# Optimization experiments

Measured on AMD Instinct MI355X. Metric: run time of the kernel, lower is better.

Reference implementation:

```python
import jax, jax.numpy as jnp
import numpy as np

EPS = 1e-10

def norm_t(x, axis):
    # zero-mean + L2 normalize along `axis` (standard NCC normalization)
    xc = x - jnp.mean(x, axis=axis, keepdims=True)
    return xc / (jnp.linalg.norm(xc, axis=axis, keepdims=True) + EPS)

def setup_inputs() -> dict:
    key = jax.random.key(0)
    k1, k2 = jax.random.split(key)
    input_compressed = jax.random.normal(k1, (1, 16, 131072), dtype=jnp.float32)  # [B, K, N]
    cmat = jax.random.normal(k2, (16, 1024), dtype=jnp.float32)                   # [K, D]
    return {"input_compressed": input_compressed, "cmat": cmat}

def reference(input_compressed, cmat):
    a = norm_t(input_compressed, axis=-2)          # [B, K, N], normalized over K
    b = norm_t(cmat, axis=0)                       # [K, D],    normalized over K
    ncc = jnp.einsum('bkn,kd->bnd', a, b)          # [B, N, D] correlation volume
    # torch: argmax(transpose(ncc,-2,-1), dim=-2) -> argmax over D -> [B, N]
    pred_depths = jnp.argmax(ncc, axis=-1)         # [B, N] int depth-bin indices
    return pred_depths
```

## Files before the change

kernel.cpp:

```cpp
#include <hip/hip_runtime.h>
#include <hip/hip_bf16.h>
#include <math.h>

#define N_PTS  131072
#define K_DIM  16
#define D_BINS 1024
#define MARGIN 1e-4f

typedef short bf16x8 __attribute__((ext_vector_type(8)));
typedef float f32x4  __attribute__((ext_vector_type(4)));

#define WS_OFF_BN    64
#define WS_OFF_B1    (WS_OFF_BN + 65536)
#define WS_OFF_B2    (WS_OFF_B1 + 32768)
#define WS_OFF_ZERO  (WS_OFF_B2 + 32768)
#define WS_OFF_WL    (WS_OFF_ZERO + 16)
#define WS_NEED      (WS_OFF_WL + 4 * N_PTS)

__device__ __forceinline__ void norm_np(const float* __restrict__ p,
                                        int stride, int n, float* __restrict__ a) {
#pragma clang fp contract(off)
    float v[K_DIM];
#pragma unroll
    for (int k = 0; k < K_DIM; ++k) v[k] = p[(size_t)k * stride + n];
    float s = v[0];
#pragma unroll
    for (int k = 1; k < K_DIM; ++k) s = s + v[k];
    const float mean = s / 16.0f;
    float sq[K_DIM];
#pragma unroll
    for (int k = 0; k < K_DIM; ++k) { a[k] = v[k] - mean; sq[k] = a[k] * a[k]; }
    float ss = sq[0];
#pragma unroll
    for (int k = 1; k < K_DIM; ++k) ss = ss + sq[k];
    const float denom = sqrtf(ss) + 1e-10f;
#pragma unroll
    for (int k = 0; k < K_DIM; ++k) a[k] = a[k] / denom;
}

__device__ __forceinline__ unsigned short bf16_bits(float f) {
    __hip_bfloat16 h = __float2bfloat16(f);
    unsigned short u;
    __builtin_memcpy(&u, &h, 2);
    return u;
}
__device__ __forceinline__ float bf16_val(float f) {
    return __bfloat162float(__float2bfloat16(f));
}

__global__ __launch_bounds__(256) void prep_b(
    const float* __restrict__ cmat, float* __restrict__ bnT,
    unsigned short* __restrict__ B1, unsigned short* __restrict__ B2,
    unsigned short* __restrict__ zblk, int* __restrict__ wl_count) {
#pragma clang fp contract(off)
    if (blockIdx.x == 0) {
        if (threadIdx.x == 0) *wl_count = 0;
        if (threadIdx.x < 8) zblk[threadIdx.x] = 0;
    }
    const int d = blockIdx.x * 256 + threadIdx.x;
    if (d >= D_BINS) return;

    float t[K_DIM];
    norm_np(cmat, D_BINS, d, t);

    const int tile = d >> 4, n = d & 15;
#pragma unroll
    for (int k = 0; k < K_DIM; ++k) {
        bnT[d * K_DIM + k] = t[k];
        const float hi_f = bf16_val(t[k]);
        const int idx = tile * 256 + ((k >> 3) * 16 + n) * 8 + (k & 7);
        B1[idx] = bf16_bits(t[k]);
        B2[idx] = bf16_bits(t[k] - hi_f);
    }
}

__global__ __launch_bounds__(256) void mfma_screen(
    const float* __restrict__ x, const unsigned short* __restrict__ B1,
    const unsigned short* __restrict__ B2, const unsigned short* __restrict__ zblk,
    int* __restrict__ out, int* __restrict__ wl, int* __restrict__ wl_count) {
#pragma clang fp contract(off)
    const int lane = threadIdx.x & 63;
    const int wv   = threadIdx.x >> 6;
    const int W    = blockIdx.x * 4 + wv;
    const int P    = W * 64;
    const int m    = lane & 15;
    const int q    = lane >> 4;

    bf16x8 A[4];
#pragma unroll
    for (int t = 0; t < 4; ++t) {
        float a[K_DIM];
        norm_np(x, N_PTS, P + t * 16 + m, a);
        unsigned short els[8];
#pragma unroll
        for (int j = 0; j < 8; ++j) {
            const int k = (q & 1) * 8 + j;
            if (q < 2) els[j] = bf16_bits(a[k]);
            else       els[j] = bf16_bits(a[k] - bf16_val(a[k]));
        }
        __builtin_memcpy(&A[t], els, 16);
    }

    float b1v[4][4], b2v[4][4];
    int   i1v[4][4];
#pragma unroll
    for (int t = 0; t < 4; ++t)
#pragma unroll
        for (int r = 0; r < 4; ++r) {
            b1v[t][r] = -3.402823466e38f; b2v[t][r] = -3.402823466e38f;
            i1v[t][r] = 0;
        }

    const unsigned short* b1p = B1 + (size_t)(lane & 31) * 8;
    const unsigned short* b2p = (lane < 32) ? (B2 + (size_t)lane * 8) : zblk;
    const int b2s = (lane < 32) ? 256 : 0;

    for (int i = 0; i < 64; ++i) {
        bf16x8 bf1, bf2;
        __builtin_memcpy(&bf1, b1p + (size_t)i * 256, 16);
        __builtin_memcpy(&bf2, b2p + (size_t)i * b2s, 16);

        f32x4 acc[4];
#pragma unroll
        for (int t = 0; t < 4; ++t)
            acc[t] = __builtin_amdgcn_mfma_f32_16x16x32_bf16(
                A[t], bf1, (f32x4){0.f, 0.f, 0.f, 0.f}, 0, 0, 0);
#pragma unroll
        for (int t = 0; t < 4; ++t)
            acc[t] = __builtin_amdgcn_mfma_f32_16x16x32_bf16(
                A[t], bf2, acc[t], 0, 0, 0);

        const int d = i * 16 + m;
#pragma unroll
        for (int t = 0; t < 4; ++t)
#pragma unroll
            for (int r = 0; r < 4; ++r) {
                const float sc = acc[t][r];
                if (sc > b1v[t][r]) { b2v[t][r] = b1v[t][r]; b1v[t][r] = sc; i1v[t][r] = d; }
                else                 b2v[t][r] = fmaxf(b2v[t][r], sc);
            }
    }

#pragma unroll
    for (int t = 0; t < 4; ++t)
#pragma unroll
        for (int r = 0; r < 4; ++r) {
            float B1v = b1v[t][r], B2v = b2v[t][r];
            int   I1  = i1v[t][r];
#pragma unroll
            for (int s = 1; s <= 8; s <<= 1) {
                const float ob1 = __shfl_xor(B1v, s, 16);
                const float ob2 = __shfl_xor(B2v, s, 16);
                const int   oi  = __shfl_xor(I1,  s, 16);
                if (ob1 > B1v || (ob1 == B1v && oi < I1)) {
                    B2v = fmaxf(B1v, ob2); B1v = ob1; I1 = oi;
                } else {
                    B2v = fmaxf(B2v, ob1);
                }
            }
            if (m == 0) {
                const int p = P + t * 16 + q * 4 + r;
                if (B1v - B2v > MARGIN) {
                    out[p] = I1;
                } else {
                    const int pos = atomicAdd(wl_count, 1);
                    wl[pos] = p;
                }
            }
        }
}

__global__ __launch_bounds__(256) void ncc_exact_refine(
    const float* __restrict__ x, const float* __restrict__ bnT,
    int* __restrict__ out, const int* __restrict__ wl,
    const int* __restrict__ wl_count) {
#pragma clang fp contract(off)
    const int count  = *wl_count;
    const int lane   = threadIdx.x & 63;
    const int wave   = (blockIdx.x * 256 + threadIdx.x) >> 6;
    const int nwaves = (gridDim.x * 256) >> 6;

    for (int i = wave; i < count; i += nwaves) {
        const int n = wl[i];
        float a[K_DIM];
        norm_np(x, N_PTS, n, a);

        float best = -3.402823466e38f;
        int   idx  = 0x7fffffff;
        const float4* b4 = (const float4*)bnT;
        for (int t = 0; t < 16; ++t) {
            const int d = t * 64 + lane;
            const float4 q0 = b4[d * 4 + 0];
            const float4 q1 = b4[d * 4 + 1];
            const float4 q2 = b4[d * 4 + 2];
            const float4 q3 = b4[d * 4 + 3];
            float sc;
            sc = a[0] * q0.x;
            sc = sc + a[1]  * q0.y; sc = sc + a[2]  * q0.z; sc = sc + a[3]  * q0.w;
            sc = sc + a[4]  * q1.x; sc = sc + a[5]  * q1.y; sc = sc + a[6]  * q1.z;
            sc = sc + a[7]  * q1.w; sc = sc + a[8]  * q2.x; sc = sc + a[9]  * q2.y;
            sc = sc + a[10] * q2.z; sc = sc + a[11] * q2.w; sc = sc + a[12] * q3.x;
            sc = sc + a[13] * q3.y; sc = sc + a[14] * q3.z; sc = sc + a[15] * q3.w;
            if (sc > best) { best = sc; idx = d; }
        }
#pragma unroll
        for (int mk = 1; mk <= 32; mk <<= 1) {
            const float ob = __shfl_xor(best, mk);
            const int   oi = __shfl_xor(idx,  mk);
            if (ob > best || (ob == best && oi < idx)) { best = ob; idx = oi; }
        }
        if (lane == 0) out[n] = idx;
    }
}

__global__ __launch_bounds__(256) void ncc_argmax_np32(
    const float* __restrict__ x, const float* __restrict__ bnT,
    int* __restrict__ out) {
#pragma clang fp contract(off)
    const int n = blockIdx.x * 256 + threadIdx.x;
    float a[K_DIM];
    norm_np(x, N_PTS, n, a);

    float best = -3.402823466e38f;
    int   idx  = 0;
    const float4* b4 = (const float4*)bnT;
#pragma unroll 2
    for (int d = 0; d < D_BINS; ++d) {
        const float4 q0 = b4[d * 4 + 0];
        const float4 q1 = b4[d * 4 + 1];
        const float4 q2 = b4[d * 4 + 2];
        const float4 q3 = b4[d * 4 + 3];
        float sc;
        sc = a[0] * q0.x;
        sc = sc + a[1]  * q0.y; sc = sc + a[2]  * q0.z; sc = sc + a[3]  * q0.w;
        sc = sc + a[4]  * q1.x; sc = sc + a[5]  * q1.y; sc = sc + a[6]  * q1.z;
        sc = sc + a[7]  * q1.w; sc = sc + a[8]  * q2.x; sc = sc + a[9]  * q2.y;
        sc = sc + a[10] * q2.z; sc = sc + a[11] * q2.w; sc = sc + a[12] * q3.x;
        sc = sc + a[13] * q3.y; sc = sc + a[14] * q3.z; sc = sc + a[15] * q3.w;
        if (sc > best) { best = sc; idx = d; }
    }
    out[n] = idx;
}

__global__ __launch_bounds__(256) void normalize_rows_only(
    const float* __restrict__ cmat, float* __restrict__ bnT) {
#pragma clang fp contract(off)
    const int d = blockIdx.x * 256 + threadIdx.x;
    if (d >= D_BINS) return;
    float t[K_DIM];
    norm_np(cmat, D_BINS, d, t);
#pragma unroll
    for (int k = 0; k < K_DIM; ++k) bnT[d * K_DIM + k] = t[k];
}

extern "C" void kernel_launch(void* const* d_in, const int* in_sizes, int n_in,
                              void* d_out, int out_size, void* d_ws, size_t ws_size,
                              hipStream_t stream) {
    const float* x    = (const float*)d_in[0];
    const float* cmat = (const float*)d_in[1];
    int* out = (int*)d_out;
    char* ws = (char*)d_ws;

    if (ws_size >= (size_t)WS_NEED) {
        int*            wl_count = (int*)ws;
        float*          bnT      = (float*)(ws + WS_OFF_BN);
        unsigned short* B1       = (unsigned short*)(ws + WS_OFF_B1);
        unsigned short* B2       = (unsigned short*)(ws + WS_OFF_B2);
        unsigned short* zblk     = (unsigned short*)(ws + WS_OFF_ZERO);
        int*            wl       = (int*)(ws + WS_OFF_WL);

        prep_b<<<4, 256, 0, stream>>>(cmat, bnT, B1, B2, zblk, wl_count);
        mfma_screen<<<512, 256, 0, stream>>>(x, B1, B2, zblk, out, wl, wl_count);
        ncc_exact_refine<<<256, 256, 0, stream>>>(x, bnT, out, wl, wl_count);
    } else {
        float* bnT = (float*)(ws + WS_OFF_BN);
        normalize_rows_only<<<4, 256, 0, stream>>>(cmat, bnT);
        ncc_argmax_np32<<<512, 256, 0, stream>>>(x, bnT, out);
    }
}
```

Measured before the change: 118.7 us.

## Stage B tiles in LDS and pack score+index into sortable uint for top-2

The screening kernel now copies the packed bf16 hi/lo B matrix into shared memory once per 512-thread block and reads it from LDS instead of global memory. Each wave handles 32 points instead of 64. The top-2 tracking packs a bias-shifted score with its truncated mantissa and complemented bin index into one unsigned word, so it needs only integer max/min instead of branches. The refine kernel gets a larger grid. The lost mantissa precision is covered by a wider margin (6e-4), which sends more points to the exact refine pass and adds LDS usage per block.

Result: faster. 108.8 us (-8.4%).

```diff
diff --git a/kernel.cpp b/kernel.cpp
--- a/kernel.cpp
+++ b/kernel.cpp
@@ -5,17 +5,15 @@
 #define N_PTS  131072
 #define K_DIM  16
 #define D_BINS 1024
-#define MARGIN 1e-4f
+#define MARGIN_P 6e-4f
 
 typedef short bf16x8 __attribute__((ext_vector_type(8)));
 typedef float f32x4  __attribute__((ext_vector_type(4)));
 
-#define WS_OFF_BN    64
-#define WS_OFF_B1    (WS_OFF_BN + 65536)
-#define WS_OFF_B2    (WS_OFF_B1 + 32768)
-#define WS_OFF_ZERO  (WS_OFF_B2 + 32768)
-#define WS_OFF_WL    (WS_OFF_ZERO + 16)
-#define WS_NEED      (WS_OFF_WL + 4 * N_PTS)
+#define WS_OFF_BN  64
+#define WS_OFF_B   65600
+#define WS_OFF_WL  131136
+#define WS_NEED    655424
 
 __device__ __forceinline__ void norm_np(const float* __restrict__ p,
                                         int stride, int n, float* __restrict__ a) {
@@ -50,19 +48,16 @@
 
 __global__ __launch_bounds__(256) void prep_b(
     const float* __restrict__ cmat, float* __restrict__ bnT,
-    unsigned short* __restrict__ B1, unsigned short* __restrict__ B2,
-    unsigned short* __restrict__ zblk, int* __restrict__ wl_count) {
-#pragma clang fp contract(off)
-    if (blockIdx.x == 0) {
-        if (threadIdx.x == 0) *wl_count = 0;
-        if (threadIdx.x < 8) zblk[threadIdx.x] = 0;
-    }
+    unsigned short* __restrict__ B1, int* __restrict__ wl_count) {
+#pragma clang fp contract(off)
+    if (blockIdx.x == 0 && threadIdx.x == 0) *wl_count = 0;
     const int d = blockIdx.x * 256 + threadIdx.x;
     if (d >= D_BINS) return;
 
     float t[K_DIM];
     norm_np(cmat, D_BINS, d, t);
 
+    unsigned short* B2 = B1 + 16384;
     const int tile = d >> 4, n = d & 15;
 #pragma unroll
     for (int k = 0; k < K_DIM; ++k) {
@@ -74,21 +69,30 @@
     }
 }
 
-__global__ __launch_bounds__(256) void mfma_screen(
-    const float* __restrict__ x, const unsigned short* __restrict__ B1,
-    const unsigned short* __restrict__ B2, const unsigned short* __restrict__ zblk,
+__global__ __launch_bounds__(512) void mfma_screen(
+    const float* __restrict__ x, const unsigned short* __restrict__ Bpack,
     int* __restrict__ out, int* __restrict__ wl, int* __restrict__ wl_count) {
 #pragma clang fp contract(off)
+    __shared__ float4 ldsB[4097];
+
+    {
+        const float4* src = (const float4*)Bpack;
+#pragma unroll
+        for (int j = 0; j < 8; ++j)
+            ldsB[threadIdx.x + j * 512] = src[threadIdx.x + j * 512];
+        if (threadIdx.x == 0) ldsB[4096] = (float4){0.f, 0.f, 0.f, 0.f};
+    }
+
     const int lane = threadIdx.x & 63;
     const int wv   = threadIdx.x >> 6;
-    const int W    = blockIdx.x * 4 + wv;
-    const int P    = W * 64;
+    const int W    = blockIdx.x * 8 + wv;
+    const int P    = W * 32;
     const int m    = lane & 15;
     const int q    = lane >> 4;
 
-    bf16x8 A[4];
-#pragma unroll
-    for (int t = 0; t < 4; ++t) {
+    bf16x8 A[2];
+#pragma unroll
+    for (int t = 0; t < 2; ++t) {
         float a[K_DIM];
         norm_np(x, N_PTS, P + t * 16 + m, a);
         unsigned short els[8];
@@ -101,67 +105,67 @@
         __builtin_memcpy(&A[t], els, 16);
     }
 
-    float b1v[4][4], b2v[4][4];
-    int   i1v[4][4];
-#pragma unroll
-    for (int t = 0; t < 4; ++t)
-#pragma unroll
-        for (int r = 0; r < 4; ++r) {
-            b1v[t][r] = -3.402823466e38f; b2v[t][r] = -3.402823466e38f;
-            i1v[t][r] = 0;
-        }
-
-    const unsigned short* b1p = B1 + (size_t)(lane & 31) * 8;
-    const unsigned short* b2p = (lane < 32) ? (B2 + (size_t)lane * 8) : zblk;
-    const int b2s = (lane < 32) ? 256 : 0;
+    __syncthreads();
+
+    const char* lb = (const char*)ldsB;
+    const char* b1p = lb + (size_t)(lane & 31) * 16;
+    const char* b2p = (lane < 32) ? (lb + 32768 + (size_t)lane * 16) : (lb + 65536);
+    const int   b2s = (lane < 32) ? 512 : 0;
+
+    unsigned ub1[2][4], ub2[2][4];
+#pragma unroll
+    for (int t = 0; t < 2; ++t)
+#pragma unroll
+        for (int r = 0; r < 4; ++r) { ub1[t][r] = 0u; ub2[t][r] = 0u; }
+
+    const unsigned mask = 0xFFFFF800u;
 
     for (int i = 0; i < 64; ++i) {
         bf16x8 bf1, bf2;
-        __builtin_memcpy(&bf1, b1p + (size_t)i * 256, 16);
+        __builtin_memcpy(&bf1, b1p + (size_t)i * 512, 16);
         __builtin_memcpy(&bf2, b2p + (size_t)i * b2s, 16);
 
-        f32x4 acc[4];
-#pragma unroll
-        for (int t = 0; t < 4; ++t)
+        f32x4 acc[2];
+#pragma unroll
+        for (int t = 0; t < 2; ++t)
             acc[t] = __builtin_amdgcn_mfma_f32_16x16x32_bf16(
-                A[t], bf1, (f32x4){0.f, 0.f, 0.f, 0.f}, 0, 0, 0);
-#pragma unroll
-        for (int t = 0; t < 4; ++t)
+                A[t], bf1, (f32x4){2.f, 2.f, 2.f, 2.f}, 0, 0, 0);
+#pragma unroll
+        for (int t = 0; t < 2; ++t)
             acc[t] = __builtin_amdgcn_mfma_f32_16x16x32_bf16(
                 A[t], bf2, acc[t], 0, 0, 0);
 
-        const int d = i * 16 + m;
-#pragma unroll
-        for (int t = 0; t < 4; ++t)
+        const unsigned dcomp = 2047u - (unsigned)(i * 16 + m);
+#pragma unroll
+        for (int t = 0; t < 2; ++t)
 #pragma unroll
             for (int r = 0; r < 4; ++r) {
-                const float sc = acc[t][r];
-                if (sc > b1v[t][r]) { b2v[t][r] = b1v[t][r]; b1v[t][r] = sc; i1v[t][r] = d; }
-                else                 b2v[t][r] = fmaxf(b2v[t][r], sc);
+                const unsigned u = (__float_as_uint(acc[t][r]) & mask) | dcomp;
+                const unsigned nx = max(ub1[t][r], u);
+                ub2[t][r] = max(ub2[t][r], min(ub1[t][r], u));
+                ub1[t][r] = nx;
             }
     }
 
 #pragma unroll
-    for (int t = 0; t < 4; ++t)
+    for (int t = 0; t < 2; ++t)
 #pragma unroll
         for (int r = 0; r < 4; ++r) {
-            float B1v = b1v[t][r], B2v = b2v[t][r];
-            int   I1  = i1v[t][r];
+            unsigned u1 = ub1[t][r], u2 = ub2[t][r];
 #pragma unroll
             for (int s = 1; s <= 8; s <<= 1) {
-                const float ob1 = __shfl_xor(B1v, s, 16);
-                const float ob2 = __shfl_xor(B2v, s, 16);
-                const int   oi  = __shfl_xor(I1,  s, 16);
-                if (ob1 > B1v || (ob1 == B1v && oi < I1)) {
-                    B2v = fmaxf(B1v, ob2); B1v = ob1; I1 = oi;
-                } else {
-                    B2v = fmaxf(B2v, ob1);
-                }
+                const unsigned o1 = (unsigned)__shfl_xor((int)u1, s, 16);
+                const unsigned o2 = (unsigned)__shfl_xor((int)u2, s, 16);
+                const unsigned n1 = max(u1, o1);
+                u2 = max(min(u1, o1), max(u2, o2));
+                u1 = n1;
             }
             if (m == 0) {
-                const int p = P + t * 16 + q * 4 + r;
-                if (B1v - B2v > MARGIN) {
-                    out[p] = I1;
+                const int p  = P + t * 16 + q * 4 + r;
+                const float s1 = __uint_as_float(u1 & mask);
+                const float s2 = __uint_as_float(u2 & mask);
+                if (s1 - s2 > MARGIN_P) {
+                    out[p] = 2047 - (int)(u1 & 2047u);
                 } else {
                     const int pos = atomicAdd(wl_count, 1);
                     wl[pos] = p;
@@ -264,14 +268,12 @@
     if (ws_size >= (size_t)WS_NEED) {
         int*            wl_count = (int*)ws;
         float*          bnT      = (float*)(ws + WS_OFF_BN);
-        unsigned short* B1       = (unsigned short*)(ws + WS_OFF_B1);
-        unsigned short* B2       = (unsigned short*)(ws + WS_OFF_B2);
-        unsigned short* zblk     = (unsigned short*)(ws + WS_OFF_ZERO);
+        unsigned short* Bpack    = (unsigned short*)(ws + WS_OFF_B);
         int*            wl       = (int*)(ws + WS_OFF_WL);
 
-        prep_b<<<4, 256, 0, stream>>>(cmat, bnT, B1, B2, zblk, wl_count);
-        mfma_screen<<<512, 256, 0, stream>>>(x, B1, B2, zblk, out, wl, wl_count);
-        ncc_exact_refine<<<256, 256, 0, stream>>>(x, bnT, out, wl, wl_count);
+        prep_b<<<4, 256, 0, stream>>>(cmat, bnT, Bpack, wl_count);
+        mfma_screen<<<512, 512, 0, stream>>>(x, Bpack, out, wl, wl_count);
+        ncc_exact_refine<<<512, 256, 0, stream>>>(x, bnT, out, wl, wl_count);
     } else {
         float* bnT = (float*)(ws + WS_OFF_BN);
         normalize_rows_only<<<4, 256, 0, stream>>>(cmat, bnT);
```
